# Optimization experiments

Hardware: AMD Instinct MI355X
Metric: run time of the kernel (lower is better)

## Reference

```python
import jax, jax.numpy as jnp
import numpy as np


def _grid_sample(feat, grid):
    """Bilinear grid_sample, zeros padding, align_corners=False (torch default).
    feat: (B,C,H,W); grid: (B,Hg,Wg,2) normalized to [-1,1]. Returns (B,C,Hg,Wg)."""
    B, C, H, W = feat.shape
    gx, gy = grid[..., 0], grid[..., 1]
    ix = ((gx + 1.0) * W - 1.0) * 0.5
    iy = ((gy + 1.0) * H - 1.0) * 0.5
    x0 = jnp.floor(ix)
    y0 = jnp.floor(iy)
    wx = ix - x0
    wy = iy - y0

    def sample_one(f, x0, y0, wx, wy):
        def gather(xi, yi):
            valid = (xi >= 0) & (xi <= W - 1) & (yi >= 0) & (yi <= H - 1)
            xc = jnp.clip(xi, 0, W - 1).astype(jnp.int32)
            yc = jnp.clip(yi, 0, H - 1).astype(jnp.int32)
            return f[:, yc, xc] * valid[None].astype(f.dtype)
        v00 = gather(x0, y0)
        v01 = gather(x0 + 1, y0)
        v10 = gather(x0, y0 + 1)
        v11 = gather(x0 + 1, y0 + 1)
        return (v00 * (1 - wx) * (1 - wy) + v01 * wx * (1 - wy)
                + v10 * (1 - wx) * wy + v11 * wx * wy)

    return jax.vmap(sample_one)(feat, x0, y0, wx, wy)


def _homo_warp(src_feat, depth_hypo, src_K, src_c2w, ref_K, ref_c2w):
    """src_feat (B,C,H,W), depth_hypo (B,D,H,W) -> warped (B,C,D,H,W)."""
    B, C, H, W = src_feat.shape
    D = depth_hypo.shape[1]
    src_w2c = jnp.linalg.inv(src_c2w)
    ref_w2c = jnp.linalg.inv(ref_c2w)
    # Faithful to torch: clone w2c, overwrite top-left 3x3 with intrinsics.
    src_K4 = src_w2c.at[:, :3, :3].set(src_K)
    ref_K4 = ref_w2c.at[:, :3, :3].set(ref_K)
    src_proj = src_K4 @ src_w2c
    ref_proj = ref_K4 @ ref_w2c
    proj = src_proj @ jnp.linalg.inv(ref_proj)
    rot = proj[:, :3, :3]                      # (B,3,3)
    trans = proj[:, :3, 3]                     # (B,3)
    y, x = jnp.meshgrid(jnp.arange(H, dtype=src_feat.dtype),
                        jnp.arange(W, dtype=src_feat.dtype), indexing='ij')
    xyz = jnp.stack([x.ravel(), y.ravel(), jnp.ones(H * W, src_feat.dtype)], 0)  # (3,HW)
    rot_xyz = jnp.einsum('bij,jn->bin', rot, xyz)                                 # (B,3,HW)
    d = depth_hypo.reshape(B, 1, D, H * W)
    proj_xyz = rot_xyz[:, :, None, :] * d + trans[:, :, None, None]               # (B,3,D,HW)
    proj_xy = proj_xyz[:, :2] / proj_xyz[:, 2:3]
    gx = proj_xy[:, 0] / ((W - 1) / 2.0) - 1.0
    gy = proj_xy[:, 1] / ((H - 1) / 2.0) - 1.0
    grid = jax.lax.stop_gradient(jnp.stack([gx, gy], -1).reshape(B, D * H, W, 2))
    warped = _grid_sample(src_feat, grid)                                          # (B,C,D*H,W)
    return warped.reshape(B, C, D, H, W)


def _unfold5(x):
    """F.unfold(k=5,p=2) reshaped: (B,C,H,W) -> (B,C,25,H,W); k = dy*5+dx."""
    B, C, H, W = x.shape
    xp = jnp.pad(x, ((0, 0), (0, 0), (2, 2), (2, 2)))
    return jnp.stack([xp[:, :, dy:dy + H, dx:dx + W]
                      for dy in range(5) for dx in range(5)], axis=2)


def _cost_aggregation(cost, ref_feat, depth_hypo):
    B, D, H, W = cost.shape
    CENTER = 12  # index of 5x5 window center
    cost_nb = _unfold5(cost)                                           # (B,D,25,H,W)
    depth_nb = jax.lax.stop_gradient(_unfold5(depth_hypo))             # (B,D,25,H,W)
    w_depth = jax.nn.softmax(-jnp.abs(depth_nb - depth_nb[:, :, CENTER:CENTER + 1]), axis=2)
    feat_nb = jax.lax.stop_gradient(_unfold5(ref_feat))                # (B,C,25,H,W)
    w_feat = jnp.sum(feat_nb[:, :, CENTER:CENTER + 1] * feat_nb, axis=1, keepdims=True)
    w_feat = jax.nn.softmax(jnp.broadcast_to(w_feat, (B, D, 25, H, W)), axis=2)
    weight = jax.lax.stop_gradient(jax.nn.softmax(w_depth * w_feat, axis=2))
    return jnp.sum(cost_nb * weight, axis=2)                           # (B,D,H,W)


def setup_inputs() -> dict:
    key = jax.random.key(0)
    V, B, C, D, H, W = 3, 2, 32, 32, 128, 160
    k1, k2 = jax.random.split(key)
    features = jax.random.normal(k1, (V, B, C, H, W), jnp.float32)
    uncertainty = jax.random.normal(k2, (B, H, W), jnp.float32)
    K = np.array([[float(W), 0.0, (W - 1) / 2.0],
                  [0.0, float(W), (H - 1) / 2.0],
                  [0.0, 0.0, 1.0]], np.float32)
    intrinsics = np.broadcast_to(K, (V, B, 3, 3)).copy()
    c2w = np.tile(np.eye(4, dtype=np.float32), (V, B, 1, 1))
    for v in range(1, V):
        ang = 0.05 * v
        R = np.array([[np.cos(ang), 0.0, np.sin(ang)],
                      [0.0, 1.0, 0.0],
                      [-np.sin(ang), 0.0, np.cos(ang)]], np.float32)
        c2w[v, :, :3, :3] = R
        c2w[v, :, 0, 3] = 0.2 * v
    depth_vals = jnp.asarray(np.linspace(2.0, 10.0, D, dtype=np.float32))
    depth_hypo = jnp.broadcast_to(depth_vals[None, :, None, None], (B, D, H, W)) + 0.0
    return {
        'features': features,
        'intrinsics': jnp.asarray(intrinsics),
        'cam_to_world': jnp.asarray(c2w),
        'depth_hypo': depth_hypo,
        'uncertainty': uncertainty,
    }


def reference(features, intrinsics, cam_to_world, depth_hypo, uncertainty):
    ref_feat = features[0]                                             # (B,C,H,W)
    V = features.shape[0]
    unc = jax.nn.sigmoid(uncertainty)[:, None, None]                   # (B,1,1,H,W)
    pairwise = []
    for v in range(1, V):
        warped = _homo_warp(features[v], depth_hypo,
                            intrinsics[v], cam_to_world[v],
                            intrinsics[0], cam_to_world[0])            # (B,C,D,H,W)
        c = jnp.sum(ref_feat[:, :, None] * warped, axis=1, keepdims=True)  # correlation
        pairwise.append(c * unc)
    cost = jnp.min(jnp.stack(pairwise, 0), axis=0)[:, 0]               # (B,D,H,W)
    agg = _cost_aggregation(cost, ref_feat, depth_hypo)
    prob = jax.nn.softmax(agg, axis=1)
    return jnp.sum(prob * depth_hypo, axis=1)                          # (B,H,W)
```

## Files before the change

kernel.cpp:

```cpp
#include <hip/hip_runtime.h>
#include <hip/hip_fp16.h>
#include <math.h>

#define V_ 3
#define B_ 2
#define C_ 32
#define D_ 32
#define H_ 128
#define W_ 160
#define HW_ (H_*W_)
#define NPIX_ (B_*H_*W_)
#define NCOST_ (B_*D_*H_*W_)

struct H8 { __half2 h[4]; };

__device__ __forceinline__ void inv4(const double* m, double* o) {
    double inv[16];
    inv[0]  =  m[5]*m[10]*m[15] - m[5]*m[11]*m[14] - m[9]*m[6]*m[15] + m[9]*m[7]*m[14] + m[13]*m[6]*m[11] - m[13]*m[7]*m[10];
    inv[4]  = -m[4]*m[10]*m[15] + m[4]*m[11]*m[14] + m[8]*m[6]*m[15] - m[8]*m[7]*m[14] - m[12]*m[6]*m[11] + m[12]*m[7]*m[10];
    inv[8]  =  m[4]*m[9]*m[15]  - m[4]*m[11]*m[13] - m[8]*m[5]*m[15] + m[8]*m[7]*m[13] + m[12]*m[5]*m[11] - m[12]*m[7]*m[9];
    inv[12] = -m[4]*m[9]*m[14]  + m[4]*m[10]*m[13] + m[8]*m[5]*m[14] - m[8]*m[6]*m[13] - m[12]*m[5]*m[10] + m[12]*m[6]*m[9];
    inv[1]  = -m[1]*m[10]*m[15] + m[1]*m[11]*m[14] + m[9]*m[2]*m[15] - m[9]*m[3]*m[14] - m[13]*m[2]*m[11] + m[13]*m[3]*m[10];
    inv[5]  =  m[0]*m[10]*m[15] - m[0]*m[11]*m[14] - m[8]*m[2]*m[15] + m[8]*m[3]*m[14] + m[12]*m[2]*m[11] - m[12]*m[3]*m[10];
    inv[9]  = -m[0]*m[9]*m[15]  + m[0]*m[11]*m[13] + m[8]*m[1]*m[15] - m[8]*m[3]*m[13] - m[12]*m[1]*m[11] + m[12]*m[3]*m[9];
    inv[13] =  m[0]*m[9]*m[14]  - m[0]*m[10]*m[13] - m[8]*m[1]*m[14] + m[8]*m[2]*m[13] + m[12]*m[1]*m[10] - m[12]*m[2]*m[9];
    inv[2]  =  m[1]*m[6]*m[15]  - m[1]*m[7]*m[14]  - m[5]*m[2]*m[15] + m[5]*m[3]*m[14] + m[13]*m[2]*m[7]  - m[13]*m[3]*m[6];
    inv[6]  = -m[0]*m[6]*m[15]  + m[0]*m[7]*m[14]  + m[4]*m[2]*m[15] - m[4]*m[3]*m[14] - m[12]*m[2]*m[7]  + m[12]*m[3]*m[6];
    inv[10] =  m[0]*m[5]*m[15]  - m[0]*m[7]*m[13]  - m[4]*m[1]*m[15] + m[4]*m[3]*m[13] + m[12]*m[1]*m[7]  - m[12]*m[3]*m[5];
    inv[14] = -m[0]*m[5]*m[14]  + m[0]*m[6]*m[13]  + m[4]*m[1]*m[14] - m[4]*m[2]*m[13] - m[12]*m[1]*m[6]  + m[12]*m[2]*m[5];
    inv[3]  = -m[1]*m[6]*m[11]  + m[1]*m[7]*m[10]  + m[5]*m[2]*m[11] - m[5]*m[3]*m[10] - m[9]*m[2]*m[7]   + m[9]*m[3]*m[6];
    inv[7]  =  m[0]*m[6]*m[11]  - m[0]*m[7]*m[10]  - m[4]*m[2]*m[11] + m[4]*m[3]*m[10] + m[8]*m[2]*m[7]   - m[8]*m[3]*m[6];
    inv[11] = -m[0]*m[5]*m[11]  + m[0]*m[7]*m[9]   + m[4]*m[1]*m[11] - m[4]*m[3]*m[9]  - m[8]*m[1]*m[7]   + m[8]*m[3]*m[5];
    inv[15] =  m[0]*m[5]*m[10]  - m[0]*m[6]*m[9]   - m[4]*m[1]*m[10] + m[4]*m[2]*m[9]  + m[8]*m[1]*m[6]   - m[8]*m[2]*m[5];
    double det = m[0]*inv[0] + m[1]*inv[4] + m[2]*inv[8] + m[3]*inv[12];
    det = 1.0 / det;
    for (int i = 0; i < 16; i++) o[i] = inv[i] * det;
}

__device__ __forceinline__ void mm4(const double* A, const double* Bm, double* Cm) {
    for (int r = 0; r < 4; r++)
        for (int c = 0; c < 4; c++) {
            double s = 0.0;
            for (int k = 0; k < 4; k++) s += A[r*4+k] * Bm[k*4+c];
            Cm[r*4+c] = s;
        }
}

__global__ void proj_kernel(const float* __restrict__ K, const float* __restrict__ c2w,
                            float* __restrict__ proj_out) {
    int t = blockIdx.x * blockDim.x + threadIdx.x;
    if (t >= (V_-1) * B_) return;
    int vv = t / B_;
    int b  = t % B_;
    int v  = vv + 1;
    double sc[16], rc[16];
    for (int i = 0; i < 16; i++) {
        sc[i] = (double)c2w[((size_t)v * B_ + b) * 16 + i];
        rc[i] = (double)c2w[((size_t)0 * B_ + b) * 16 + i];
    }
    double sw[16], rw[16];
    inv4(sc, sw);
    inv4(rc, rw);
    double sK[16], rK[16];
    for (int i = 0; i < 16; i++) { sK[i] = sw[i]; rK[i] = rw[i]; }
    for (int r = 0; r < 3; r++)
        for (int c = 0; c < 3; c++) {
            sK[r*4+c] = (double)K[((size_t)v * B_ + b) * 9 + r*3 + c];
            rK[r*4+c] = (double)K[((size_t)0 * B_ + b) * 9 + r*3 + c];
        }
    double sp[16], rp[16], rpi[16], P[16];
    mm4(sK, sw, sp);
    mm4(rK, rw, rp);
    inv4(rp, rpi);
    mm4(sp, rpi, P);
    float* o = proj_out + (size_t)t * 12;
    for (int r = 0; r < 3; r++)
        for (int c = 0; c < 3; c++) o[r*3+c] = (float)P[r*4+c];
    for (int r = 0; r < 3; r++) o[9+r] = (float)P[r*4+3];
}

__global__ void __launch_bounds__(256) transpose_kernel(const float* __restrict__ feat,
                                                        float* __restrict__ refT,
                                                        __half* __restrict__ fh) {
    __shared__ float lds[32][33];
    int bid = blockIdx.x;
    int xt = bid % (W_ / 32);
    int y  = (bid / (W_ / 32)) % H_;
    int vb = bid / ((W_ / 32) * H_);
    int v = vb >> 1, b = vb & 1;
    int x0 = xt * 32;
    int tid = threadIdx.x;
    int xl = tid & 31;
    int ch = tid >> 5;
#pragma unroll
    for (int it = 0; it < 4; it++) {
        int c = it * 8 + ch;
        lds[c][xl] = feat[((size_t)(vb * C_ + c) * H_ + y) * W_ + x0 + xl];
    }
    __syncthreads();
    int c4 = tid & 7;
    int xw = tid >> 3;
    float4 o;
    o.x = lds[c4*4+0][xw];
    o.y = lds[c4*4+1][xw];
    o.z = lds[c4*4+2][xw];
    o.w = lds[c4*4+3][xw];
    size_t pix = (size_t)(b * H_ + y) * W_ + x0 + xw;
    if (v == 0) {
        *(float4*)(refT + pix * C_ + c4 * 4) = o;
    } else {
        uint2 st;
        __half2 p0 = __floats2half2_rn(o.x, o.y);
        __half2 p1 = __floats2half2_rn(o.z, o.w);
        st.x = *(unsigned int*)&p0;
        st.y = *(unsigned int*)&p1;
        size_t dst = ((size_t)((v - 1) * B_ + b) * HW_ + (y * W_ + x0 + xw));
        *(uint2*)((unsigned short*)fh + dst * C_ + c4 * 4) = st;
    }
}

__global__ void __launch_bounds__(256, 4) cost_kernel(const float* __restrict__ refT,
                                                      const __half* __restrict__ fh,
                                                      const float* __restrict__ depth,
                                                      const float* __restrict__ unc,
                                                      const float* __restrict__ proj,
                                                      float* __restrict__ cost) {
    __shared__ float4 lw[2][256];
    __shared__ int4   lo[2][256];
    int tid = threadIdx.x;
    const int blocksPerDt = NPIX_ / 32;
    int dt      = blockIdx.x / blocksPerDt;
    int pixbase = (blockIdx.x % blocksPerDt) * 32;
    int d0 = dt * 8;

    {
        int pixl = tid & 31;
        int dl   = tid >> 5;
        int pix = pixbase + pixl;
        int x = pix % W_;
        int y = (pix / W_) % H_;
        int b = pix / HW_;
        float dep = depth[((b * D_ + d0 + dl) * H_ + y) * W_ + x];
        float fx = (float)x, fy = (float)y;
#pragma unroll
        for (int v = 0; v < 2; v++) {
            const float* P = proj + ((size_t)v * B_ + b) * 12;
            float rx = P[0]*fx + P[1]*fy + P[2];
            float ry = P[3]*fx + P[4]*fy + P[5];
            float rz = P[6]*fx + P[7]*fy + P[8];
            float px = rx * dep + P[9];
            float py = ry * dep + P[10];
            float pz = rz * dep + P[11];
            float inv_pz = 1.0f / pz;
            float t0 = px * inv_pz;
            float t1 = py * inv_pz;
            float gx = t0 / ((W_ - 1) * 0.5f) - 1.0f;
            float gy = t1 / ((H_ - 1) * 0.5f) - 1.0f;
            float ix = ((gx + 1.0f) * W_ - 1.0f) * 0.5f;
            float iy = ((gy + 1.0f) * H_ - 1.0f) * 0.5f;
            float x0f = floorf(ix), y0f = floorf(iy);
            float wx = ix - x0f, wy = iy - y0f;
            int x0 = (int)x0f, y0 = (int)y0f;
            int x1 = x0 + 1, y1 = y0 + 1;
            bool vx0 = (x0 >= 0) && (x0 <= W_ - 1);
            bool vx1 = (x1 >= 0) && (x1 <= W_ - 1);
            bool vy0 = (y0 >= 0) && (y0 <= H_ - 1);
            bool vy1 = (y1 >= 0) && (y1 <= H_ - 1);
            float4 w;
            w.x = (vx0 && vy0) ? (1.0f - wx) * (1.0f - wy) : 0.0f;
            w.y = (vx1 && vy0) ? wx * (1.0f - wy) : 0.0f;
            w.z = (vx0 && vy1) ? (1.0f - wx) * wy : 0.0f;
            w.w = (vx1 && vy1) ? wx * wy : 0.0f;
            int xc0 = min(max(x0, 0), W_ - 1), xc1 = min(max(x1, 0), W_ - 1);
            int yc0 = min(max(y0, 0), H_ - 1), yc1 = min(max(y1, 0), H_ - 1);
            int4 o;
            o.x = yc0 * W_ + xc0;
            o.y = yc0 * W_ + xc1;
            o.z = yc1 * W_ + xc0;
            o.w = yc1 * W_ + xc1;
            lw[v][tid] = w;
            lo[v][tid] = o;
        }
    }
    __syncthreads();

    int c8 = tid & 3;
    int g  = (tid >> 2) & 31;
    int h  = tid >> 7;
    int pix = pixbase + g;
    int x = pix % W_;
    int y = (pix / W_) % H_;
    int b = pix / HW_;

    const float4* rT4 = (const float4*)refT;
    const float4 r0 = rT4[(size_t)pix * 8 + c8 * 2];
    const float4 r1 = rT4[(size_t)pix * 8 + c8 * 2 + 1];
    const H8* fh8 = (const H8*)fh;
    size_t baseA = ((size_t)(0 * B_ + b) * HW_) * 4 + c8;
    size_t baseB = ((size_t)(1 * B_ + b) * HW_) * 4 + c8;

    float u = unc[pix];
    float sig = 1.0f / (1.0f + __expf(-u));

    float myres = 0.0f;
#pragma unroll
    for (int i = 0; i < 4; i++) {
        int e = (h * 4 + i) * 32 + g;
        float pv[2];
#pragma unroll
        for (int v = 0; v < 2; v++) {
            float4 Wt = lw[v][e];
            int4   Of = lo[v][e];
            size_t base = v ? baseB : baseA;
            H8 a  = fh8[base + (size_t)Of.x * 4];
            H8 bq = fh8[base + (size_t)Of.y * 4];
            H8 cq = fh8[base + (size_t)Of.z * 4];
            H8 eq = fh8[base + (size_t)Of.w * 4];
            __half2 w0 = __float2half2_rn(Wt.x);
            __half2 w1 = __float2half2_rn(Wt.y);
            __half2 w2 = __float2half2_rn(Wt.z);
            __half2 w3 = __float2half2_rn(Wt.w);
            __half2 acc0 = __hmul2(w0, a.h[0]);
            __half2 acc1 = __hmul2(w0, a.h[1]);
            __half2 acc2 = __hmul2(w0, a.h[2]);
            __half2 acc3 = __hmul2(w0, a.h[3]);
            acc0 = __hfma2(w1, bq.h[0], acc0);
            acc1 = __hfma2(w1, bq.h[1], acc1);
            acc2 = __hfma2(w1, bq.h[2], acc2);
            acc3 = __hfma2(w1, bq.h[3], acc3);
            acc0 = __hfma2(w2, cq.h[0], acc0);
            acc1 = __hfma2(w2, cq.h[1], acc1);
            acc2 = __hfma2(w2, cq.h[2], acc2);
            acc3 = __hfma2(w2, cq.h[3], acc3);
            acc0 = __hfma2(w3, eq.h[0], acc0);
            acc1 = __hfma2(w3, eq.h[1], acc1);
            acc2 = __hfma2(w3, eq.h[2], acc2);
            acc3 = __hfma2(w3, eq.h[3], acc3);
            float2 f0 = __half22float2(acc0);
            float2 f1 = __half22float2(acc1);
            float2 f2 = __half22float2(acc2);
            float2 f3 = __half22float2(acc3);
            float p = r0.x*f0.x + r0.y*f0.y + r0.z*f1.x + r0.w*f1.y
                    + r1.x*f2.x + r1.y*f2.y + r1.z*f3.x + r1.w*f3.y;
            p += __shfl_xor(p, 1);
            p += __shfl_xor(p, 2);
            pv[v] = p;
        }
        float r = fminf(pv[0], pv[1]) * sig;
        if (c8 == i) myres = r;
    }
    cost[((b * D_ + d0 + h * 4 + c8) * H_ + y) * W_ + x] = myres;
}

#define AG_DT(arr, dd, ry, rx) arr[((dd) * 5 + (ry)) * 36 + (rx)]
__global__ void __launch_bounds__(256) aggfinal_kernel(const float* __restrict__ refT,
                                                       const float* __restrict__ depth,
                                                       const float* __restrict__ cost,
                                                       float* __restrict__ out) {
    __shared__ float smem[2 * D_ * 5 * 36];
    __shared__ float wf[25][32];
    __shared__ float aval[D_][32];
    int tid = threadIdx.x;
    int pixbase = blockIdx.x * 32;
    int x0 = pixbase % W_;
    int yb = (pixbase / W_) % H_;
    int b  = pixbase / HW_;

    {
        float4* wbox = (float4*)smem;
        const float4* rT4 = (const float4*)refT;
        for (int e = tid; e < 5 * 36 * 8; e += 256) {
            int ent = e >> 3, q = e & 7;
            int ry = ent / 36, rx = ent - ry * 36;
            int yy = yb + ry - 2, xx = x0 + rx - 2;
            float4 val = make_float4(0.f, 0.f, 0.f, 0.f);
            if (yy >= 0 && yy < H_ && xx >= 0 && xx < W_)
                val = rT4[(size_t)((b * H_ + yy) * W_ + xx) * 8 + q];
            wbox[e] = val;
        }
        __syncthreads();

        int g  = tid >> 3;
        int c4 = tid & 7;
        const float4 r = wbox[(2 * 36 + g + 2) * 8 + c4];
        float logit[25];
#pragma unroll
        for (int k = 0; k < 25; k++) {
            int dy = k / 5, dx = k % 5;
            float4 q = wbox[(dy * 36 + g + dx) * 8 + c4];
            float p = r.x*q.x + r.y*q.y + r.z*q.z + r.w*q.w;
            p += __shfl_xor(p, 1);
            p += __shfl_xor(p, 2);
            p += __shfl_xor(p, 4);
            logit[k] = p;
        }
        float m = logit[0];
#pragma unroll
        for (int k = 1; k < 25; k++) m = fmaxf(m, logit[k]);
        float s = 0.0f;
#pragma unroll
        for (int k = 0; k < 25; k++) { logit[k] = __expf(logit[k] - m); s += logit[k]; }
        float inv_s = 1.0f / s;
#pragma unroll
        for (int t = 0; t < 3; t++) {
            int k = c4 + 8 * t;
            wf[k][g] = logit[k] * inv_s;
        }
        if (c4 == 0) wf[24][g] = logit[24] * inv_s;
        __syncthreads();
    }

    float* dtile = smem;
    float* ctile = smem + D_ * 5 * 36;
    for (int li = tid; li < D_ * 5 * 36; li += 256) {
        int dd  = li / 180;
        int rem = li - dd * 180;
        int ry  = rem / 36;
        int rx  = rem - ry * 36;
        int yy = yb + ry - 2;
        int xx = x0 + rx - 2;
        bool ok = (yy >= 0) && (yy < H_) && (xx >= 0) && (xx < W_);
        size_t gidx = ((size_t)(b * D_ + dd) * H_ + yy) * W_ + xx;
        dtile[li] = ok ? depth[gidx] : 0.0f;
        ctile[li] = ok ? cost[gidx]  : 0.0f;
    }
    __syncthreads();

    int p    = tid & 31;
    int dgrp = tid >> 5;
#pragma unroll
    for (int i = 0; i < 4; i++) {
        int d = dgrp * 4 + i;
        float dc = AG_DT(dtile, d, 2, p + 2);

        float wd[25];
        float m1 = -1e30f;
#pragma unroll
        for (int k = 0; k < 25; k++) {
            int dy = k / 5, dx = k % 5;
            float nd = AG_DT(dtile, d, dy, p + dx);
            float l = -fabsf(nd - dc);
            wd[k] = l;
            m1 = fmaxf(m1, l);
        }
        float s1 = 0.0f;
#pragma unroll
        for (int k = 0; k < 25; k++) { wd[k] = __expf(wd[k] - m1); s1 += wd[k]; }
        float inv_s1 = 1.0f / s1;

        float lg[25];
        float m2 = -1e30f;
#pragma unroll
        for (int k = 0; k < 25; k++) {
            float l = (wd[k] * inv_s1) * wf[k][p];
            lg[k] = l;
            m2 = fmaxf(m2, l);
        }
        float s2 = 0.0f;
        float acc = 0.0f;
#pragma unroll
        for (int k = 0; k < 25; k++) {
            float e = __expf(lg[k] - m2);
            s2 += e;
            int dy = k / 5, dx = k % 5;
            acc += AG_DT(ctile, d, dy, p + dx) * e;
        }
        aval[d][p] = acc / s2;
    }
    __syncthreads();

    if (tid < 32) {
        float m = -1e30f;
#pragma unroll
        for (int dd = 0; dd < D_; dd++) m = fmaxf(m, aval[dd][tid]);
        float s = 0.0f, ws = 0.0f;
#pragma unroll
        for (int dd = 0; dd < D_; dd++) {
            float e = __expf(aval[dd][tid] - m);
            s += e;
            ws += e * AG_DT(dtile, dd, 2, tid + 2);
        }
        out[pixbase + tid] = ws / s;
    }
}

extern "C" void kernel_launch(void* const* d_in, const int* in_sizes, int n_in,
                              void* d_out, int out_size, void* d_ws, size_t ws_size,
                              hipStream_t stream) {
    const float* features = (const float*)d_in[0];
    const float* intr     = (const float*)d_in[1];
    const float* c2w      = (const float*)d_in[2];
    const float* depth    = (const float*)d_in[3];
    const float* unc      = (const float*)d_in[4];
    float* out = (float*)d_out;

    float*  ws    = (float*)d_ws;
    float*  refT  = ws;
    __half* fh    = (__half*)(refT + (size_t)B_ * HW_ * C_);
    float*  cost  = (float*)(fh + (size_t)2 * B_ * HW_ * C_);
    float*  proj  = cost + NCOST_;

    hipLaunchKernelGGL(proj_kernel, dim3(1), dim3(64), 0, stream, intr, c2w, proj);
    hipLaunchKernelGGL(transpose_kernel, dim3(V_ * B_ * H_ * (W_ / 32)), dim3(256), 0, stream,
                       features, refT, fh);
    hipLaunchKernelGGL(cost_kernel, dim3((NPIX_ * 4) / 32), dim3(256), 0, stream,
                       refT, fh, depth, unc, proj, cost);
    hipLaunchKernelGGL(aggfinal_kernel, dim3(NPIX_ / 32), dim3(256), 0, stream,
                       refT, depth, cost, out);
}
```

Before: 85.27 us.

## Tile aggregation kernel as 8x4 2D pixel blocks with padded feature box

Changes the aggregation kernel's block tile from a 32x1 row strip to an 8x4 2D patch. This cuts the halo loaded per block from 5x36 to 8x12 entries for the depth, cost and feature tiles, reducing global traffic and shared-memory footprint. The feature box also gets a stride of 9 float4 per entry to reduce LDS bank conflicts. In exchange the shared-tile index math and output addressing become more complex, and global reads per row become shorter, less coalesced segments.

```diff
diff --git a/kernel.cpp b/kernel.cpp
--- a/kernel.cpp
+++ b/kernel.cpp
@@ -252,42 +252,48 @@
     cost[((b * D_ + d0 + h * 4 + c8) * H_ + y) * W_ + x] = myres;
 }
 
-#define AG_DT(arr, dd, ry, rx) arr[((dd) * 5 + (ry)) * 36 + (rx)]
+#define TX_ 8
+#define TY_ 4
+#define AG(arr, dd, ry, rx) arr[((((dd) * 8 + (ry)) << 4) + (rx))]
 __global__ void __launch_bounds__(256) aggfinal_kernel(const float* __restrict__ refT,
                                                        const float* __restrict__ depth,
                                                        const float* __restrict__ cost,
                                                        float* __restrict__ out) {
-    __shared__ float smem[2 * D_ * 5 * 36];
+    __shared__ float smem[2 * D_ * 8 * 16];
     __shared__ float wf[25][32];
     __shared__ float aval[D_][32];
     int tid = threadIdx.x;
-    int pixbase = blockIdx.x * 32;
-    int x0 = pixbase % W_;
-    int yb = (pixbase / W_) % H_;
-    int b  = pixbase / HW_;
+    int bid = blockIdx.x;
+    const int XT = W_ / TX_;
+    int xt = bid % XT;
+    int yt = (bid / XT) % (H_ / TY_);
+    int b  = bid / (XT * (H_ / TY_));
+    int x0 = xt * TX_;
+    int yb = yt * TY_;
 
     {
         float4* wbox = (float4*)smem;
         const float4* rT4 = (const float4*)refT;
-        for (int e = tid; e < 5 * 36 * 8; e += 256) {
+        for (int e = tid; e < 8 * 12 * 8; e += 256) {
             int ent = e >> 3, q = e & 7;
-            int ry = ent / 36, rx = ent - ry * 36;
+            int ry = ent / 12, rx = ent - ry * 12;
             int yy = yb + ry - 2, xx = x0 + rx - 2;
             float4 val = make_float4(0.f, 0.f, 0.f, 0.f);
             if (yy >= 0 && yy < H_ && xx >= 0 && xx < W_)
                 val = rT4[(size_t)((b * H_ + yy) * W_ + xx) * 8 + q];
-            wbox[e] = val;
+            wbox[ent * 9 + q] = val;
         }
         __syncthreads();
 
         int g  = tid >> 3;
         int c4 = tid & 7;
-        const float4 r = wbox[(2 * 36 + g + 2) * 8 + c4];
+        int px = g & 7, py = g >> 3;
+        const float4 r = wbox[((py + 2) * 12 + px + 2) * 9 + c4];
         float logit[25];
 #pragma unroll
         for (int k = 0; k < 25; k++) {
             int dy = k / 5, dx = k % 5;
-            float4 q = wbox[(dy * 36 + g + dx) * 8 + c4];
+            float4 q = wbox[((py + dy) * 12 + px + dx) * 9 + c4];
             float p = r.x*q.x + r.y*q.y + r.z*q.z + r.w*q.w;
             p += __shfl_xor(p, 1);
             p += __shfl_xor(p, 2);
@@ -311,34 +317,35 @@
     }
 
     float* dtile = smem;
-    float* ctile = smem + D_ * 5 * 36;
-    for (int li = tid; li < D_ * 5 * 36; li += 256) {
-        int dd  = li / 180;
-        int rem = li - dd * 180;
-        int ry  = rem / 36;
-        int rx  = rem - ry * 36;
+    float* ctile = smem + D_ * 8 * 16;
+    for (int li = tid; li < D_ * 8 * 12; li += 256) {
+        int dd  = li / 96;
+        int rem = li - dd * 96;
+        int ry  = rem / 12;
+        int rx  = rem - ry * 12;
         int yy = yb + ry - 2;
         int xx = x0 + rx - 2;
         bool ok = (yy >= 0) && (yy < H_) && (xx >= 0) && (xx < W_);
         size_t gidx = ((size_t)(b * D_ + dd) * H_ + yy) * W_ + xx;
-        dtile[li] = ok ? depth[gidx] : 0.0f;
-        ctile[li] = ok ? cost[gidx]  : 0.0f;
+        AG(dtile, dd, ry, rx) = ok ? depth[gidx] : 0.0f;
+        AG(ctile, dd, ry, rx) = ok ? cost[gidx]  : 0.0f;
     }
     __syncthreads();
 
     int p    = tid & 31;
+    int px = p & 7, py = p >> 3;
     int dgrp = tid >> 5;
 #pragma unroll
     for (int i = 0; i < 4; i++) {
         int d = dgrp * 4 + i;
-        float dc = AG_DT(dtile, d, 2, p + 2);
+        float dc = AG(dtile, d, py + 2, px + 2);
 
         float wd[25];
         float m1 = -1e30f;
 #pragma unroll
         for (int k = 0; k < 25; k++) {
             int dy = k / 5, dx = k % 5;
-            float nd = AG_DT(dtile, d, dy, p + dx);
+            float nd = AG(dtile, d, py + dy, px + dx);
             float l = -fabsf(nd - dc);
             wd[k] = l;
             m1 = fmaxf(m1, l);
@@ -363,13 +370,14 @@
             float e = __expf(lg[k] - m2);
             s2 += e;
             int dy = k / 5, dx = k % 5;
-            acc += AG_DT(ctile, d, dy, p + dx) * e;
+            acc += AG(ctile, d, dy + py, dx + px) * e;
         }
         aval[d][p] = acc / s2;
     }
     __syncthreads();
 
     if (tid < 32) {
+        int qx = tid & 7, qy = tid >> 3;
         float m = -1e30f;
 #pragma unroll
         for (int dd = 0; dd < D_; dd++) m = fmaxf(m, aval[dd][tid]);
@@ -378,9 +386,9 @@
         for (int dd = 0; dd < D_; dd++) {
             float e = __expf(aval[dd][tid] - m);
             s += e;
-            ws += e * AG_DT(dtile, dd, 2, tid + 2);
-        }
-        out[pixbase + tid] = ws / s;
+            ws += e * AG(dtile, dd, qy + 2, qx + 2);
+        }
+        out[(b * H_ + yb + qy) * W_ + x0 + qx] = ws / s;
     }
 }
 
@@ -405,6 +413,6 @@
                        features, refT, fh);
     hipLaunchKernelGGL(cost_kernel, dim3((NPIX_ * 4) / 32), dim3(256), 0, stream,
                        refT, fh, depth, unc, proj, cost);
-    hipLaunchKernelGGL(aggfinal_kernel, dim3(NPIX_ / 32), dim3(256), 0, stream,
+    hipLaunchKernelGGL(aggfinal_kernel, dim3(NPIX_ / (TX_ * TY_)), dim3(256), 0, stream,
                        refT, depth, cost, out);
 }
```

Measured after the change: 82.22 us. 3.6% less time.
